# Kernel tuning notes

Measured on AMD Instinct MI355X. Metric: run time of the kernel, lower is better.

The kernel has to match this reference:

```python
import jax, jax.numpy as jnp
import numpy as np

EPS = 1e-5  # BatchNorm eps; fresh module eval => running_mean=0, running_var=1


def _cbr(t, W, g, b):
    # 1x1 conv (no bias) over [B,C,L] + BatchNorm2d(eval, mean0/var1) + ReLU
    t = jnp.einsum('oc,bcl->bol', W, t)
    t = t * (g / jnp.sqrt(1.0 + EPS))[None, :, None] + b[None, :, None]
    return jax.nn.relu(t)


def _wavelet(y):
    # SFP.wavelet: chunk channels into 3; for chunk i (1-based) take the level-i
    # haar wavedec approximation coeffs along axis 2 and mean-reduce them.
    # For even lengths, level-i haar approx = block-sum over 2^i samples * 2^(-i/2).
    B, C, L = y.shape
    parts = jnp.split(y, 3, axis=1)
    zs = []
    for i, k in enumerate(parts, start=1):
        s = 2 ** i
        a = k.reshape(B, C // 3, L // s, s).sum(-1) * (2.0 ** (-i / 2))  # [B,C/3,L/2^i]
        zs.append(a.mean(axis=2))
    return jnp.concatenate(zs, axis=1)  # [B,C]


def setup_inputs() -> dict:
    key = jax.random.key(0)
    ks = jax.random.split(key, 16)
    B, C, H, W = 32, 384, 64, 64
    R = C // 16
    f = lambda k, sh, s=0.05: jax.random.normal(k, sh, jnp.float32) * s
    u = lambda k, sh: jax.random.uniform(k, sh, jnp.float32, 0.5, 1.5)
    return dict(
        x=jax.random.normal(ks[0], (B, C, H, W), jnp.float32),
        Wy=f(ks[1], (C, C)), gy=u(ks[2], (C,)), by=f(ks[3], (C,)),
        Wh=f(ks[4], (C, C)), gh=u(ks[5], (C,)), bh=f(ks[6], (C,)),
        Ww=f(ks[7], (C, C)), gw=u(ks[8], (C,)), bw=f(ks[9], (C,)),
        fc0_w=f(ks[10], (R, C)), fc0_b=f(ks[11], (R,)),
        bn1_g=u(ks[12], (R,)), bn1_b=f(ks[13], (R,)),
        fc1_w=f(ks[14], (C, R)), fc1_b=f(ks[15], (C,)),
    )


def reference(x, Wy, gy, by, Wh, gh, bh, Ww, gw, bw,
              fc0_w, fc0_b, bn1_g, bn1_b, fc1_w, fc1_b):
    B, C, H, Wd = x.shape
    # CoordPooling: mean over width -> [B,C,H]; mean over height -> [B,C,W]; cat along coord axis
    y = jnp.concatenate([x.mean(axis=3), x.mean(axis=2)], axis=2)  # [B,C,H+W]
    y = _cbr(y, Wy, gy, by)
    xh = _cbr(y[:, :, :H], Wh, gh, bh)   # [B,C,H]
    xw = _cbr(y[:, :, H:], Ww, gw, bw)   # [B,C,W]
    # SFP channel gate (torch detaches y before the wavelet)
    z = _wavelet(jax.lax.stop_gradient(y))          # [B,C]
    z = z @ fc0_w.T + fc0_b                          # [B,C/16]
    z = jax.nn.relu(z * (bn1_g / jnp.sqrt(1.0 + EPS)) + bn1_b)
    z = z @ fc1_w.T + fc1_b                          # [B,C]
    gate = jax.nn.sigmoid(xh[:, :, :, None] * xw[:, :, None, :])  # [B,C,H,W]
    return x * gate + x * z[:, :, None, None]
```

## Files before the change

### kernel.cpp

```cpp
#include <hip/hip_runtime.h>
#include <math.h>

#define RSQ 0.99999500003749975f

typedef __attribute__((ext_vector_type(8))) __bf16 bf16x8;
typedef __attribute__((ext_vector_type(4))) float f32x4;
typedef __attribute__((ext_vector_type(4))) unsigned int u32x4;
typedef __attribute__((ext_vector_type(2))) unsigned int u32x2;

__device__ __forceinline__ unsigned short bfb(float v) {
    return __builtin_bit_cast(unsigned short, (__bf16)v);
}
__device__ __forceinline__ float bff(unsigned short u) {
    unsigned int x = ((unsigned int)u) << 16;
    return __builtin_bit_cast(float, x);
}

__global__ __launch_bounds__(256) void kpool(const float* __restrict__ x,
                                             const float* __restrict__ Wy,
                                             const float* __restrict__ Wh,
                                             const float* __restrict__ Ww,
                                             unsigned short* __restrict__ ypb,
                                             unsigned short* __restrict__ Wp) {
    __shared__ float sm[6208];
    int bid = blockIdx.x;
    int t = threadIdx.x;
    if (bid >= 12288) {
        int e = bid - 12288;
        int m = e / 24, ot = e % 24;
        const float* W = (m == 0) ? Wy : (m == 1) ? Wh : Ww;
#pragma unroll
        for (int k = 0; k < 6; ++k) {
            int idx = t + k * 256;
            int r = idx / 96, c4 = idx % 96;
            f32x4 v = *reinterpret_cast<const f32x4*>(W + (size_t)(ot * 16 + r) * 384 + c4 * 4);
            *reinterpret_cast<f32x4*>(&sm[r * 388 + c4 * 4]) = v;
        }
        __syncthreads();
#pragma unroll
        for (int k = 0; k < 3; ++k) {
            int idx = t + k * 256;
            int cs = idx >> 6, j = idx & 63;
            const float* src = &sm[(j & 15) * 388 + cs * 32 + (j >> 4) * 8];
            u32x4 pk;
            pk.x = (unsigned int)bfb(src[0]) | ((unsigned int)bfb(src[1]) << 16);
            pk.y = (unsigned int)bfb(src[2]) | ((unsigned int)bfb(src[3]) << 16);
            pk.z = (unsigned int)bfb(src[4]) | ((unsigned int)bfb(src[5]) << 16);
            pk.w = (unsigned int)bfb(src[6]) | ((unsigned int)bfb(src[7]) << 16);
            *reinterpret_cast<u32x4*>(Wp + ((size_t)(m * 24 + ot) * 12 + cs) * 512 + j * 8) = pk;
        }
        return;
    }
    float* pl = sm;
    float* part = sm + 4096;
    const f32x4* xp = reinterpret_cast<const f32x4*>(x) + (size_t)bid * 1024;
    f32x4* pl4 = reinterpret_cast<f32x4*>(pl);
#pragma unroll
    for (int k = 0; k < 4; ++k) pl4[k * 256 + t] = __builtin_nontemporal_load(xp + k * 256 + t);
    __syncthreads();
    int lane = t & 63, pt = t >> 6;
    float rs = 0.f;
#pragma unroll
    for (int j = 0; j < 16; ++j) {
        int w = (pt * 16 + j + lane) & 63;
        rs += pl[lane * 64 + w];
    }
    part[t] = rs;
    __syncthreads();
    if (t < 64) {
        float v = part[t] + part[t + 64] + part[t + 128] + part[t + 192];
        ypb[(size_t)bid * 128 + t] = bfb(v * 0.015625f);
    }
    __syncthreads();
    float cs = 0.f;
#pragma unroll
    for (int j = 0; j < 16; ++j) cs += pl[(pt * 16 + j) * 64 + lane];
    part[t] = cs;
    __syncthreads();
    if (t < 64) {
        float v = part[t] + part[t + 64] + part[t + 128] + part[t + 192];
        ypb[(size_t)bid * 128 + 64 + t] = bfb(v * 0.015625f);
    }
}

__global__ __launch_bounds__(256) void kcbr1(const unsigned short* __restrict__ yp,
    const unsigned short* __restrict__ Wp,
    const float* __restrict__ g, const float* __restrict__ bb,
    unsigned short* __restrict__ yT) {
    __shared__ unsigned short Bs[2][2048];
    int bid = blockIdx.x;
    int t = threadIdx.x;
    int ot = bid % 6, lt = (bid / 6) % 4, b = bid / 24;
    int o0 = ot * 64, l0 = lt * 32;
    int w = t >> 6, lane = t & 63;

    int c_s0 = t >> 3,            l4_0 = (t & 7) * 4;
    int c_s1 = (t + 256) >> 3,    l4_1 = l4_0;
    const unsigned short* ypbase = yp + (size_t)b * 49152 + l0;
    const unsigned short* Asrc = Wp + (size_t)(ot * 4 + w) * 12 * 512 + lane * 8;

    f32x4 acc0 = {0.f, 0.f, 0.f, 0.f};
    f32x4 acc1 = {0.f, 0.f, 0.f, 0.f};

    auto stage = [&](int buf, u32x2 r0, u32x2 r1) {
        unsigned short* B0 = &Bs[buf][(c_s0 >> 3) * 256 + l4_0 * 8 + (c_s0 & 7)];
        B0[0]  = (unsigned short)(r0.x & 0xffff);
        B0[8]  = (unsigned short)(r0.x >> 16);
        B0[16] = (unsigned short)(r0.y & 0xffff);
        B0[24] = (unsigned short)(r0.y >> 16);
        unsigned short* B1 = &Bs[buf][(c_s1 >> 3) * 256 + l4_1 * 8 + (c_s1 & 7)];
        B1[0]  = (unsigned short)(r1.x & 0xffff);
        B1[8]  = (unsigned short)(r1.x >> 16);
        B1[16] = (unsigned short)(r1.y & 0xffff);
        B1[24] = (unsigned short)(r1.y >> 16);
    };
    auto ldB = [&](int ch, u32x2& r0, u32x2& r1) {
        r0 = *reinterpret_cast<const u32x2*>(ypbase + (size_t)(ch * 64 + c_s0) * 128 + l4_0);
        r1 = *reinterpret_cast<const u32x2*>(ypbase + (size_t)(ch * 64 + c_s1) * 128 + l4_1);
    };

    u32x2 r0, r1;
    ldB(0, r0, r1);
    stage(0, r0, r1);
#pragma unroll
    for (int ch = 0; ch < 6; ++ch) {
        __syncthreads();
        if (ch < 5) ldB(ch + 1, r0, r1);
        const unsigned short* Bb = Bs[ch & 1];
        int li = lane & 15, hi = lane >> 4;
#pragma unroll
        for (int kk = 0; kk < 2; ++kk) {
            bf16x8 av = *reinterpret_cast<const bf16x8*>(Asrc + (size_t)(ch * 2 + kk) * 512);
            int cg = kk * 4 + hi;
            bf16x8 bv0 = *reinterpret_cast<const bf16x8*>(&Bb[cg * 256 + li * 8]);
            bf16x8 bv1 = *reinterpret_cast<const bf16x8*>(&Bb[cg * 256 + (li + 16) * 8]);
            acc0 = __builtin_amdgcn_mfma_f32_16x16x32_bf16(av, bv0, acc0, 0, 0, 0);
            acc1 = __builtin_amdgcn_mfma_f32_16x16x32_bf16(av, bv1, acc1, 0, 0, 0);
        }
        if (ch < 5) stage((ch + 1) & 1, r0, r1);
    }
    int oB = o0 + w * 16 + (lane >> 4) * 4;
    int lB = l0 + (lane & 15);
    float s0 = g[oB] * RSQ,     bi0 = bb[oB];
    float s1 = g[oB + 1] * RSQ, bi1 = bb[oB + 1];
    float s2 = g[oB + 2] * RSQ, bi2 = bb[oB + 2];
    float s3 = g[oB + 3] * RSQ, bi3 = bb[oB + 3];
    u32x2 p0, p1;
    p0.x = (unsigned int)bfb(fmaxf(fmaf(acc0[0], s0, bi0), 0.f)) |
           ((unsigned int)bfb(fmaxf(fmaf(acc0[1], s1, bi1), 0.f)) << 16);
    p0.y = (unsigned int)bfb(fmaxf(fmaf(acc0[2], s2, bi2), 0.f)) |
           ((unsigned int)bfb(fmaxf(fmaf(acc0[3], s3, bi3), 0.f)) << 16);
    p1.x = (unsigned int)bfb(fmaxf(fmaf(acc1[0], s0, bi0), 0.f)) |
           ((unsigned int)bfb(fmaxf(fmaf(acc1[1], s1, bi1), 0.f)) << 16);
    p1.y = (unsigned int)bfb(fmaxf(fmaf(acc1[2], s2, bi2), 0.f)) |
           ((unsigned int)bfb(fmaxf(fmaf(acc1[3], s3, bi3), 0.f)) << 16);
    *reinterpret_cast<u32x2*>(yT + ((size_t)b * 128 + lB) * 384 + oB) = p0;
    *reinterpret_cast<u32x2*>(yT + ((size_t)b * 128 + lB + 16) * 384 + oB) = p1;
}

__global__ __launch_bounds__(256, 3) void kcbr2(const unsigned short* __restrict__ yT,
    const unsigned short* __restrict__ Wp,
    const float* __restrict__ gh, const float* __restrict__ bh,
    const float* __restrict__ gw, const float* __restrict__ bw,
    float* __restrict__ hw,
    const float* __restrict__ fc0_w, const float* __restrict__ fc0_b,
    const float* __restrict__ bn1_g, const float* __restrict__ bn1_b,
    const float* __restrict__ fc1_w, const float* __restrict__ fc1_b,
    float* __restrict__ z2) {
    int bid = blockIdx.x;
    int t = threadIdx.x;
    if (bid >= 768) {
        __shared__ float z0[384];
        __shared__ float z1[24];
        int b = bid - 768;
        const unsigned short* yb = yT + (size_t)b * 49152;
        if (t < 192) {
            int c2 = t * 2;
            float s0 = 0.f, s1 = 0.f;
#pragma unroll 8
            for (int l = 0; l < 128; ++l) {
                unsigned int v = *reinterpret_cast<const unsigned int*>(yb + (size_t)l * 384 + c2);
                s0 += bff((unsigned short)(v & 0xffff));
                s1 += bff((unsigned short)(v >> 16));
            }
            float fac = (c2 < 128) ? 1.41421356237310f : (c2 < 256 ? 2.0f : 2.82842712474619f);
            z0[c2]     = s0 * (fac * 0.0078125f);
            z0[c2 + 1] = s1 * (fac * 0.0078125f);
        }
        __syncthreads();
        if (t < 96) {
            int r = t >> 2, j = t & 3;
            float p = 0.f;
            for (int c = j; c < 384; c += 4) p = fmaf(z0[c], fc0_w[r * 384 + c], p);
            p += __shfl_xor(p, 1);
            p += __shfl_xor(p, 2);
            if (j == 0) z1[r] = fmaxf(fmaf(p + fc0_b[r], bn1_g[r] * RSQ, bn1_b[r]), 0.f);
        }
        __syncthreads();
        for (int c = t; c < 384; c += 256) {
            float a = fc1_b[c];
#pragma unroll
            for (int r = 0; r < 24; ++r) a = fmaf(z1[r], fc1_w[c * 24 + r], a);
            z2[b * 384 + c] = a;
        }
        return;
    }
    int ot = bid % 6, lt = (bid / 6) % 4, b = bid / 24;
    int o0 = ot * 64, l0 = lt * 32;
    int m = (lt >= 2) ? 2 : 1;
    const float* g  = (lt >= 2) ? gw : gh;
    const float* bb = (lt >= 2) ? bw : bh;
    int w = t >> 6, lane = t & 63;
    int li = lane & 15, hi = lane >> 4;
    const unsigned short* Asrc = Wp + (size_t)(m * 24 + ot * 4 + w) * 12 * 512 + lane * 8;
    const unsigned short* B0 = yT + ((size_t)b * 128 + l0 + li) * 384 + hi * 8;
    const unsigned short* B1 = B0 + (size_t)16 * 384;

    f32x4 acc0 = {0.f, 0.f, 0.f, 0.f};
    f32x4 acc1 = {0.f, 0.f, 0.f, 0.f};
    bf16x8 av  = *reinterpret_cast<const bf16x8*>(Asrc);
    bf16x8 bv0 = *reinterpret_cast<const bf16x8*>(B0);
    bf16x8 bv1 = *reinterpret_cast<const bf16x8*>(B1);
    for (int ch = 0; ch < 12; ++ch) {
        bf16x8 avn, bv0n, bv1n;
        if (ch < 11) {
            avn  = *reinterpret_cast<const bf16x8*>(Asrc + (size_t)(ch + 1) * 512);
            bv0n = *reinterpret_cast<const bf16x8*>(B0 + (ch + 1) * 32);
            bv1n = *reinterpret_cast<const bf16x8*>(B1 + (ch + 1) * 32);
        }
        acc0 = __builtin_amdgcn_mfma_f32_16x16x32_bf16(av, bv0, acc0, 0, 0, 0);
        acc1 = __builtin_amdgcn_mfma_f32_16x16x32_bf16(av, bv1, acc1, 0, 0, 0);
        av = avn; bv0 = bv0n; bv1 = bv1n;
    }
    int oB = o0 + w * 16 + hi * 4;
    int lB = l0 + li;
#pragma unroll
    for (int r = 0; r < 4; ++r) {
        int o = oB + r;
        float sc = g[o] * RSQ, bi = bb[o];
        size_t base = ((size_t)b * 384 + o) * 128 + lB;
        hw[base]      = fmaxf(fmaf(acc0[r], sc, bi), 0.f);
        hw[base + 16] = fmaxf(fmaf(acc1[r], sc, bi), 0.f);
    }
}

__global__ __launch_bounds__(256) void kfinal(const float* __restrict__ x,
    const float* __restrict__ hw, const float* __restrict__ z2,
    float* __restrict__ out) {
    const f32x4* x4 = reinterpret_cast<const f32x4*>(x);
    f32x4* o4 = reinterpret_cast<f32x4*>(out);
    const int total4 = 12582912;
    int stride = gridDim.x * blockDim.x;
    for (int idx = blockIdx.x * blockDim.x + threadIdx.x; idx < total4; idx += stride) {
        int w4 = idx & 15;
        int h  = (idx >> 4) & 63;
        int bc = idx >> 10;
        f32x4 xv = __builtin_nontemporal_load(x4 + idx);
        float  a  = hw[(bc << 7) + h];
        const f32x4 wv = reinterpret_cast<const f32x4*>(hw)[(bc << 5) + 16 + w4];
        float  zv = z2[bc];
        f32x4 ov;
        ov.x = xv.x * (1.f / (1.f + __expf(-a * wv.x)) + zv);
        ov.y = xv.y * (1.f / (1.f + __expf(-a * wv.y)) + zv);
        ov.z = xv.z * (1.f / (1.f + __expf(-a * wv.z)) + zv);
        ov.w = xv.w * (1.f / (1.f + __expf(-a * wv.w)) + zv);
        __builtin_nontemporal_store(ov, o4 + idx);
    }
}

extern "C" void kernel_launch(void* const* d_in, const int* in_sizes, int n_in,
                              void* d_out, int out_size, void* d_ws, size_t ws_size,
                              hipStream_t stream) {
    const float* x     = (const float*)d_in[0];
    const float* Wy    = (const float*)d_in[1];
    const float* gy    = (const float*)d_in[2];
    const float* by    = (const float*)d_in[3];
    const float* Wh    = (const float*)d_in[4];
    const float* gh    = (const float*)d_in[5];
    const float* bh    = (const float*)d_in[6];
    const float* Ww    = (const float*)d_in[7];
    const float* gw    = (const float*)d_in[8];
    const float* bw    = (const float*)d_in[9];
    const float* fc0_w = (const float*)d_in[10];
    const float* fc0_b = (const float*)d_in[11];
    const float* bn1_g = (const float*)d_in[12];
    const float* bn1_b = (const float*)d_in[13];
    const float* fc1_w = (const float*)d_in[14];
    const float* fc1_b = (const float*)d_in[15];
    float* out = (float*)d_out;

    char* ws = (char*)d_ws;
    unsigned short* ypb = (unsigned short*)ws;
    unsigned short* yT  = (unsigned short*)(ws + 3145728);
    float*          hw  = (float*)(ws + 6291456);
    float*          z2  = (float*)(ws + 12582912);
    unsigned short* Wp  = (unsigned short*)(ws + 12632064);

    kpool<<<dim3(12288 + 72), dim3(256), 0, stream>>>(x, Wy, Wh, Ww, ypb, Wp);
    kcbr1<<<dim3(768), dim3(256), 0, stream>>>(ypb, Wp, gy, by, yT);
    kcbr2<<<dim3(800), dim3(256), 0, stream>>>(yT, Wp, gh, bh, gw, bw, hw,
        fc0_w, fc0_b, bn1_g, bn1_b, fc1_w, fc1_b, z2);
    kfinal<<<dim3(2048), dim3(256), 0, stream>>>(x, hw, z2, out);
}
```

Before: 140.2 us.

## Fuse all four stages into one cooperative persistent kernel with grid syncs

```diff
diff --git a/kernel.cpp b/kernel.cpp
--- a/kernel.cpp
+++ b/kernel.cpp
@@ -1,5 +1,8 @@
 #include <hip/hip_runtime.h>
+#include <hip/hip_cooperative_groups.h>
 #include <math.h>
+
+namespace cg = cooperative_groups;
 
 #define RSQ 0.99999500003749975f
 
@@ -14,6 +17,262 @@
 __device__ __forceinline__ float bff(unsigned short u) {
     unsigned int x = ((unsigned int)u) << 16;
     return __builtin_bit_cast(float, x);
+}
+
+__global__ __launch_bounds__(256, 3) void fused(
+    const float* __restrict__ x,
+    const float* __restrict__ Wy, const float* __restrict__ Wh, const float* __restrict__ Ww,
+    const float* __restrict__ gy, const float* __restrict__ by,
+    const float* __restrict__ gh, const float* __restrict__ bh,
+    const float* __restrict__ gw, const float* __restrict__ bw,
+    const float* __restrict__ fc0_w, const float* __restrict__ fc0_b,
+    const float* __restrict__ bn1_g, const float* __restrict__ bn1_b,
+    const float* __restrict__ fc1_w, const float* __restrict__ fc1_b,
+    unsigned short* __restrict__ ypb,
+    unsigned short* __restrict__ yT,
+    float* __restrict__ hw,
+    float* __restrict__ z2,
+    unsigned short* __restrict__ Wp,
+    float* __restrict__ out) {
+    __shared__ __attribute__((aligned(16))) float smf[6208];
+    cg::grid_group grid = cg::this_grid();
+    const int nb = gridDim.x;
+    int bid = blockIdx.x;
+    int t = threadIdx.x;
+
+    {
+        float* pl = smf;
+        float* part = smf + 4096;
+        for (int plane = bid; plane < 12288; plane += nb) {
+            const f32x4* xp = reinterpret_cast<const f32x4*>(x) + (size_t)plane * 1024;
+            f32x4* pl4 = reinterpret_cast<f32x4*>(pl);
+#pragma unroll
+            for (int k = 0; k < 4; ++k) pl4[k * 256 + t] = xp[k * 256 + t];
+            __syncthreads();
+            int lane = t & 63, pt = t >> 6;
+            float rs = 0.f;
+#pragma unroll
+            for (int j = 0; j < 16; ++j) {
+                int w = (pt * 16 + j + lane) & 63;
+                rs += pl[lane * 64 + w];
+            }
+            part[t] = rs;
+            __syncthreads();
+            if (t < 64) {
+                float v = part[t] + part[t + 64] + part[t + 128] + part[t + 192];
+                ypb[(size_t)plane * 128 + t] = bfb(v * 0.015625f);
+            }
+            __syncthreads();
+            float cs2 = 0.f;
+#pragma unroll
+            for (int j = 0; j < 16; ++j) cs2 += pl[(pt * 16 + j) * 64 + lane];
+            part[t] = cs2;
+            __syncthreads();
+            if (t < 64) {
+                float v = part[t] + part[t + 64] + part[t + 128] + part[t + 192];
+                ypb[(size_t)plane * 128 + 64 + t] = bfb(v * 0.015625f);
+            }
+            __syncthreads();
+        }
+        for (int wu = bid; wu < 72; wu += nb) {
+            int m = wu / 24, ot = wu % 24;
+            const float* W = (m == 0) ? Wy : (m == 1) ? Wh : Ww;
+#pragma unroll
+            for (int k = 0; k < 6; ++k) {
+                int idx = t + k * 256;
+                int r = idx / 96, c4 = idx % 96;
+                f32x4 v = *reinterpret_cast<const f32x4*>(W + (size_t)(ot * 16 + r) * 384 + c4 * 4);
+                *reinterpret_cast<f32x4*>(&smf[r * 388 + c4 * 4]) = v;
+            }
+            __syncthreads();
+#pragma unroll
+            for (int k = 0; k < 3; ++k) {
+                int idx = t + k * 256;
+                int cs = idx >> 6, j = idx & 63;
+                const float* src = &smf[(j & 15) * 388 + cs * 32 + (j >> 4) * 8];
+                u32x4 pk;
+                pk.x = (unsigned int)bfb(src[0]) | ((unsigned int)bfb(src[1]) << 16);
+                pk.y = (unsigned int)bfb(src[2]) | ((unsigned int)bfb(src[3]) << 16);
+                pk.z = (unsigned int)bfb(src[4]) | ((unsigned int)bfb(src[5]) << 16);
+                pk.w = (unsigned int)bfb(src[6]) | ((unsigned int)bfb(src[7]) << 16);
+                *reinterpret_cast<u32x4*>(Wp + ((size_t)(m * 24 + ot) * 12 + cs) * 512 + j * 8) = pk;
+            }
+            __syncthreads();
+        }
+    }
+    __threadfence();
+    grid.sync();
+
+    if (bid < 768) {
+        unsigned short* Bs0 = reinterpret_cast<unsigned short*>(smf);
+        int ot = bid % 6, lt = (bid / 6) % 4, b = bid / 24;
+        int o0 = ot * 64, l0 = lt * 32;
+        int w = t >> 6, lane = t & 63;
+        int c_s0 = t >> 3, l4_0 = (t & 7) * 4;
+        int c_s1 = (t + 256) >> 3;
+        const unsigned short* ypbase = ypb + (size_t)b * 49152 + l0;
+        const unsigned short* Asrc = Wp + (size_t)(ot * 4 + w) * 12 * 512 + lane * 8;
+
+        f32x4 acc0 = {0.f, 0.f, 0.f, 0.f};
+        f32x4 acc1 = {0.f, 0.f, 0.f, 0.f};
+        u32x2 r0, r1;
+        r0 = *reinterpret_cast<const u32x2*>(ypbase + (size_t)c_s0 * 128 + l4_0);
+        r1 = *reinterpret_cast<const u32x2*>(ypbase + (size_t)c_s1 * 128 + l4_0);
+        {
+            unsigned short* B0 = &Bs0[(c_s0 >> 3) * 256 + l4_0 * 8 + (c_s0 & 7)];
+            B0[0] = (unsigned short)(r0.x & 0xffff); B0[8] = (unsigned short)(r0.x >> 16);
+            B0[16] = (unsigned short)(r0.y & 0xffff); B0[24] = (unsigned short)(r0.y >> 16);
+            unsigned short* B1 = &Bs0[(c_s1 >> 3) * 256 + l4_0 * 8 + (c_s1 & 7)];
+            B1[0] = (unsigned short)(r1.x & 0xffff); B1[8] = (unsigned short)(r1.x >> 16);
+            B1[16] = (unsigned short)(r1.y & 0xffff); B1[24] = (unsigned short)(r1.y >> 16);
+        }
+#pragma unroll
+        for (int ch = 0; ch < 6; ++ch) {
+            __syncthreads();
+            if (ch < 5) {
+                r0 = *reinterpret_cast<const u32x2*>(ypbase + (size_t)((ch + 1) * 64 + c_s0) * 128 + l4_0);
+                r1 = *reinterpret_cast<const u32x2*>(ypbase + (size_t)((ch + 1) * 64 + c_s1) * 128 + l4_0);
+            }
+            const unsigned short* Bb = Bs0 + (ch & 1) * 2048;
+            int li = lane & 15, hi = lane >> 4;
+#pragma unroll
+            for (int kk = 0; kk < 2; ++kk) {
+                bf16x8 av = *reinterpret_cast<const bf16x8*>(Asrc + (size_t)(ch * 2 + kk) * 512);
+                int cg2 = kk * 4 + hi;
+                bf16x8 bv0 = *reinterpret_cast<const bf16x8*>(&Bb[cg2 * 256 + li * 8]);
+                bf16x8 bv1 = *reinterpret_cast<const bf16x8*>(&Bb[cg2 * 256 + (li + 16) * 8]);
+                acc0 = __builtin_amdgcn_mfma_f32_16x16x32_bf16(av, bv0, acc0, 0, 0, 0);
+                acc1 = __builtin_amdgcn_mfma_f32_16x16x32_bf16(av, bv1, acc1, 0, 0, 0);
+            }
+            if (ch < 5) {
+                unsigned short* Bw = Bs0 + ((ch + 1) & 1) * 2048;
+                unsigned short* B0 = &Bw[(c_s0 >> 3) * 256 + l4_0 * 8 + (c_s0 & 7)];
+                B0[0] = (unsigned short)(r0.x & 0xffff); B0[8] = (unsigned short)(r0.x >> 16);
+                B0[16] = (unsigned short)(r0.y & 0xffff); B0[24] = (unsigned short)(r0.y >> 16);
+                unsigned short* B1 = &Bw[(c_s1 >> 3) * 256 + l4_0 * 8 + (c_s1 & 7)];
+                B1[0] = (unsigned short)(r1.x & 0xffff); B1[8] = (unsigned short)(r1.x >> 16);
+                B1[16] = (unsigned short)(r1.y & 0xffff); B1[24] = (unsigned short)(r1.y >> 16);
+            }
+        }
+        int oB = o0 + w * 16 + (lane >> 4) * 4;
+        int lB = l0 + (lane & 15);
+        float s0 = gy[oB] * RSQ, bi0 = by[oB];
+        float s1 = gy[oB + 1] * RSQ, bi1 = by[oB + 1];
+        float s2 = gy[oB + 2] * RSQ, bi2 = by[oB + 2];
+        float s3 = gy[oB + 3] * RSQ, bi3 = by[oB + 3];
+        u32x2 p0, p1;
+        p0.x = (unsigned int)bfb(fmaxf(fmaf(acc0[0], s0, bi0), 0.f)) |
+               ((unsigned int)bfb(fmaxf(fmaf(acc0[1], s1, bi1), 0.f)) << 16);
+        p0.y = (unsigned int)bfb(fmaxf(fmaf(acc0[2], s2, bi2), 0.f)) |
+               ((unsigned int)bfb(fmaxf(fmaf(acc0[3], s3, bi3), 0.f)) << 16);
+        p1.x = (unsigned int)bfb(fmaxf(fmaf(acc1[0], s0, bi0), 0.f)) |
+               ((unsigned int)bfb(fmaxf(fmaf(acc1[1], s1, bi1), 0.f)) << 16);
+        p1.y = (unsigned int)bfb(fmaxf(fmaf(acc1[2], s2, bi2), 0.f)) |
+               ((unsigned int)bfb(fmaxf(fmaf(acc1[3], s3, bi3), 0.f)) << 16);
+        *reinterpret_cast<u32x2*>(yT + ((size_t)b * 128 + lB) * 384 + oB) = p0;
+        *reinterpret_cast<u32x2*>(yT + ((size_t)b * 128 + lB + 16) * 384 + oB) = p1;
+    }
+    __threadfence();
+    grid.sync();
+
+    for (int wu = bid; wu < 800; wu += nb) {
+        if (wu < 768) {
+            int ot = wu % 6, lt = (wu / 6) % 4, b = wu / 24;
+            int o0 = ot * 64, l0 = lt * 32;
+            int m = (lt >= 2) ? 2 : 1;
+            const float* g  = (lt >= 2) ? gw : gh;
+            const float* bb = (lt >= 2) ? bw : bh;
+            int w = t >> 6, lane = t & 63;
+            int li = lane & 15, hi = lane >> 4;
+            const unsigned short* Asrc = Wp + (size_t)(m * 24 + ot * 4 + w) * 12 * 512 + lane * 8;
+            const unsigned short* B0 = yT + ((size_t)b * 128 + l0 + li) * 384 + hi * 8;
+            const unsigned short* B1 = B0 + (size_t)16 * 384;
+            f32x4 acc0 = {0.f, 0.f, 0.f, 0.f};
+            f32x4 acc1 = {0.f, 0.f, 0.f, 0.f};
+            bf16x8 av  = *reinterpret_cast<const bf16x8*>(Asrc);
+            bf16x8 bv0 = *reinterpret_cast<const bf16x8*>(B0);
+            bf16x8 bv1 = *reinterpret_cast<const bf16x8*>(B1);
+            for (int ch = 0; ch < 12; ++ch) {
+                bf16x8 avn, bv0n, bv1n;
+                if (ch < 11) {
+                    avn  = *reinterpret_cast<const bf16x8*>(Asrc + (size_t)(ch + 1) * 512);
+                    bv0n = *reinterpret_cast<const bf16x8*>(B0 + (ch + 1) * 32);
+                    bv1n = *reinterpret_cast<const bf16x8*>(B1 + (ch + 1) * 32);
+                }
+                acc0 = __builtin_amdgcn_mfma_f32_16x16x32_bf16(av, bv0, acc0, 0, 0, 0);
+                acc1 = __builtin_amdgcn_mfma_f32_16x16x32_bf16(av, bv1, acc1, 0, 0, 0);
+                av = avn; bv0 = bv0n; bv1 = bv1n;
+            }
+            int oB = o0 + w * 16 + hi * 4;
+            int lB = l0 + li;
+#pragma unroll
+            for (int r = 0; r < 4; ++r) {
+                int o = oB + r;
+                float sc = g[o] * RSQ, bi = bb[o];
+                size_t base = ((size_t)b * 384 + o) * 128 + lB;
+                hw[base]      = fmaxf(fmaf(acc0[r], sc, bi), 0.f);
+                hw[base + 16] = fmaxf(fmaf(acc1[r], sc, bi), 0.f);
+            }
+        } else {
+            float* z0 = smf;
+            float* z1 = smf + 384;
+            int b = wu - 768;
+            const unsigned short* yb = yT + (size_t)b * 49152;
+            if (t < 192) {
+                int c2 = t * 2;
+                float s0 = 0.f, s1 = 0.f;
+#pragma unroll 8
+                for (int l = 0; l < 128; ++l) {
+                    unsigned int v = *reinterpret_cast<const unsigned int*>(yb + (size_t)l * 384 + c2);
+                    s0 += bff((unsigned short)(v & 0xffff));
+                    s1 += bff((unsigned short)(v >> 16));
+                }
+                float fac = (c2 < 128) ? 1.41421356237310f : (c2 < 256 ? 2.0f : 2.82842712474619f);
+                z0[c2]     = s0 * (fac * 0.0078125f);
+                z0[c2 + 1] = s1 * (fac * 0.0078125f);
+            }
+            __syncthreads();
+            if (t < 96) {
+                int r = t >> 2, j = t & 3;
+                float p = 0.f;
+                for (int c = j; c < 384; c += 4) p = fmaf(z0[c], fc0_w[r * 384 + c], p);
+                p += __shfl_xor(p, 1);
+                p += __shfl_xor(p, 2);
+                if (j == 0) z1[r] = fmaxf(fmaf(p + fc0_b[r], bn1_g[r] * RSQ, bn1_b[r]), 0.f);
+            }
+            __syncthreads();
+            for (int c = t; c < 384; c += 256) {
+                float a = fc1_b[c];
+#pragma unroll
+                for (int r = 0; r < 24; ++r) a = fmaf(z1[r], fc1_w[c * 24 + r], a);
+                z2[b * 384 + c] = a;
+            }
+        }
+    }
+    __threadfence();
+    grid.sync();
+
+    {
+        const f32x4* x4 = reinterpret_cast<const f32x4*>(x);
+        f32x4* o4 = reinterpret_cast<f32x4*>(out);
+        const int total4 = 12582912;
+        int stride = nb * 256;
+        for (int idx = bid * 256 + t; idx < total4; idx += stride) {
+            int w4 = idx & 15;
+            int h  = (idx >> 4) & 63;
+            int bc = idx >> 10;
+            f32x4 xv = x4[idx];
+            float  a  = hw[(bc << 7) + h];
+            const f32x4 wv = reinterpret_cast<const f32x4*>(hw)[(bc << 5) + 16 + w4];
+            float  zv = z2[bc];
+            f32x4 ov;
+            ov.x = xv.x * (1.f / (1.f + __expf(-a * wv.x)) + zv);
+            ov.y = xv.y * (1.f / (1.f + __expf(-a * wv.y)) + zv);
+            ov.z = xv.z * (1.f / (1.f + __expf(-a * wv.z)) + zv);
+            ov.w = xv.w * (1.f / (1.f + __expf(-a * wv.w)) + zv);
+            __builtin_nontemporal_store(ov, o4 + idx);
+        }
+    }
 }
 
 __global__ __launch_bounds__(256) void kpool(const float* __restrict__ x,
@@ -56,7 +315,7 @@
     const f32x4* xp = reinterpret_cast<const f32x4*>(x) + (size_t)bid * 1024;
     f32x4* pl4 = reinterpret_cast<f32x4*>(pl);
 #pragma unroll
-    for (int k = 0; k < 4; ++k) pl4[k * 256 + t] = __builtin_nontemporal_load(xp + k * 256 + t);
+    for (int k = 0; k < 4; ++k) pl4[k * 256 + t] = xp[k * 256 + t];
     __syncthreads();
     int lane = t & 63, pt = t >> 6;
     float rs = 0.f;
@@ -93,47 +352,39 @@
     int ot = bid % 6, lt = (bid / 6) % 4, b = bid / 24;
     int o0 = ot * 64, l0 = lt * 32;
     int w = t >> 6, lane = t & 63;
-
-    int c_s0 = t >> 3,            l4_0 = (t & 7) * 4;
-    int c_s1 = (t + 256) >> 3,    l4_1 = l4_0;
+    int c_s0 = t >> 3, l4_0 = (t & 7) * 4;
+    int c_s1 = (t + 256) >> 3;
     const unsigned short* ypbase = yp + (size_t)b * 49152 + l0;
     const unsigned short* Asrc = Wp + (size_t)(ot * 4 + w) * 12 * 512 + lane * 8;
-
     f32x4 acc0 = {0.f, 0.f, 0.f, 0.f};
     f32x4 acc1 = {0.f, 0.f, 0.f, 0.f};
-
     auto stage = [&](int buf, u32x2 r0, u32x2 r1) {
         unsigned short* B0 = &Bs[buf][(c_s0 >> 3) * 256 + l4_0 * 8 + (c_s0 & 7)];
-        B0[0]  = (unsigned short)(r0.x & 0xffff);
-        B0[8]  = (unsigned short)(r0.x >> 16);
-        B0[16] = (unsigned short)(r0.y & 0xffff);
-        B0[24] = (unsigned short)(r0.y >> 16);
-        unsigned short* B1 = &Bs[buf][(c_s1 >> 3) * 256 + l4_1 * 8 + (c_s1 & 7)];
-        B1[0]  = (unsigned short)(r1.x & 0xffff);
-        B1[8]  = (unsigned short)(r1.x >> 16);
-        B1[16] = (unsigned short)(r1.y & 0xffff);
-        B1[24] = (unsigned short)(r1.y >> 16);
+        B0[0] = (unsigned short)(r0.x & 0xffff); B0[8] = (unsigned short)(r0.x >> 16);
+        B0[16] = (unsigned short)(r0.y & 0xffff); B0[24] = (unsigned short)(r0.y >> 16);
+        unsigned short* B1 = &Bs[buf][(c_s1 >> 3) * 256 + l4_0 * 8 + (c_s1 & 7)];
+        B1[0] = (unsigned short)(r1.x & 0xffff); B1[8] = (unsigned short)(r1.x >> 16);
+        B1[16] = (unsigned short)(r1.y & 0xffff); B1[24] = (unsigned short)(r1.y >> 16);
     };
-    auto ldB = [&](int ch, u32x2& r0, u32x2& r1) {
-        r0 = *reinterpret_cast<const u32x2*>(ypbase + (size_t)(ch * 64 + c_s0) * 128 + l4_0);
-        r1 = *reinterpret_cast<const u32x2*>(ypbase + (size_t)(ch * 64 + c_s1) * 128 + l4_1);
-    };
-
     u32x2 r0, r1;
-    ldB(0, r0, r1);
+    r0 = *reinterpret_cast<const u32x2*>(ypbase + (size_t)c_s0 * 128 + l4_0);
+    r1 = *reinterpret_cast<const u32x2*>(ypbase + (size_t)c_s1 * 128 + l4_0);
     stage(0, r0, r1);
 #pragma unroll
     for (int ch = 0; ch < 6; ++ch) {
         __syncthreads();
-        if (ch < 5) ldB(ch + 1, r0, r1);
+        if (ch < 5) {
+            r0 = *reinterpret_cast<const u32x2*>(ypbase + (size_t)((ch + 1) * 64 + c_s0) * 128 + l4_0);
+            r1 = *reinterpret_cast<const u32x2*>(ypbase + (size_t)((ch + 1) * 64 + c_s1) * 128 + l4_0);
+        }
         const unsigned short* Bb = Bs[ch & 1];
         int li = lane & 15, hi = lane >> 4;
 #pragma unroll
         for (int kk = 0; kk < 2; ++kk) {
             bf16x8 av = *reinterpret_cast<const bf16x8*>(Asrc + (size_t)(ch * 2 + kk) * 512);
-            int cg = kk * 4 + hi;
-            bf16x8 bv0 = *reinterpret_cast<const bf16x8*>(&Bb[cg * 256 + li * 8]);
-            bf16x8 bv1 = *reinterpret_cast<const bf16x8*>(&Bb[cg * 256 + (li + 16) * 8]);
+            int cg2 = kk * 4 + hi;
+            bf16x8 bv0 = *reinterpret_cast<const bf16x8*>(&Bb[cg2 * 256 + li * 8]);
+            bf16x8 bv1 = *reinterpret_cast<const bf16x8*>(&Bb[cg2 * 256 + (li + 16) * 8]);
             acc0 = __builtin_amdgcn_mfma_f32_16x16x32_bf16(av, bv0, acc0, 0, 0, 0);
             acc1 = __builtin_amdgcn_mfma_f32_16x16x32_bf16(av, bv1, acc1, 0, 0, 0);
         }
@@ -141,7 +392,7 @@
     }
     int oB = o0 + w * 16 + (lane >> 4) * 4;
     int lB = l0 + (lane & 15);
-    float s0 = g[oB] * RSQ,     bi0 = bb[oB];
+    float s0 = g[oB] * RSQ, bi0 = bb[oB];
     float s1 = g[oB + 1] * RSQ, bi1 = bb[oB + 1];
     float s2 = g[oB + 2] * RSQ, bi2 = bb[oB + 2];
     float s3 = g[oB + 3] * RSQ, bi3 = bb[oB + 3];
@@ -215,7 +466,6 @@
     const unsigned short* Asrc = Wp + (size_t)(m * 24 + ot * 4 + w) * 12 * 512 + lane * 8;
     const unsigned short* B0 = yT + ((size_t)b * 128 + l0 + li) * 384 + hi * 8;
     const unsigned short* B1 = B0 + (size_t)16 * 384;
-
     f32x4 acc0 = {0.f, 0.f, 0.f, 0.f};
     f32x4 acc1 = {0.f, 0.f, 0.f, 0.f};
     bf16x8 av  = *reinterpret_cast<const bf16x8*>(Asrc);
@@ -255,7 +505,7 @@
         int w4 = idx & 15;
         int h  = (idx >> 4) & 63;
         int bc = idx >> 10;
-        f32x4 xv = __builtin_nontemporal_load(x4 + idx);
+        f32x4 xv = x4[idx];
         float  a  = hw[(bc << 7) + h];
         const f32x4 wv = reinterpret_cast<const f32x4*>(hw)[(bc << 5) + 16 + w4];
         float  zv = z2[bc];
@@ -292,13 +542,24 @@
     char* ws = (char*)d_ws;
     unsigned short* ypb = (unsigned short*)ws;
     unsigned short* yT  = (unsigned short*)(ws + 3145728);
-    float*          hw  = (float*)(ws + 6291456);
+    float*          hww = (float*)(ws + 6291456);
     float*          z2  = (float*)(ws + 12582912);
     unsigned short* Wp  = (unsigned short*)(ws + 12632064);
 
-    kpool<<<dim3(12288 + 72), dim3(256), 0, stream>>>(x, Wy, Wh, Ww, ypb, Wp);
-    kcbr1<<<dim3(768), dim3(256), 0, stream>>>(ypb, Wp, gy, by, yT);
-    kcbr2<<<dim3(800), dim3(256), 0, stream>>>(yT, Wp, gh, bh, gw, bw, hw,
-        fc0_w, fc0_b, bn1_g, bn1_b, fc1_w, fc1_b, z2);
-    kfinal<<<dim3(2048), dim3(256), 0, stream>>>(x, hw, z2, out);
-}
+    void* args[] = {
+        (void*)&x, (void*)&Wy, (void*)&Wh, (void*)&Ww,
+        (void*)&gy, (void*)&by, (void*)&gh, (void*)&bh, (void*)&gw, (void*)&bw,
+        (void*)&fc0_w, (void*)&fc0_b, (void*)&bn1_g, (void*)&bn1_b,
+        (void*)&fc1_w, (void*)&fc1_b,
+        (void*)&ypb, (void*)&yT, (void*)&hww, (void*)&z2, (void*)&Wp, (void*)&out,
+    };
+    hipError_t err = hipLaunchCooperativeKernel((void*)fused, dim3(768), dim3(256),
+                                                args, 0, stream);
+    if (err != hipSuccess) {
+        kpool<<<dim3(12288 + 72), dim3(256), 0, stream>>>(x, Wy, Wh, Ww, ypb, Wp);
+        kcbr1<<<dim3(768), dim3(256), 0, stream>>>(ypb, Wp, gy, by, yT);
+        kcbr2<<<dim3(800), dim3(256), 0, stream>>>(yT, Wp, gh, bh, gw, bw, hww,
+            fc0_w, fc0_b, bn1_g, bn1_b, fc1_w, fc1_b, z2);
+        kfinal<<<dim3(2048), dim3(256), 0, stream>>>(x, hww, z2, out);
+    }
+}
```

Result: slower. 560.6 us (+299.8%).
